# Kernel tuning notes

Hardware: AMD Instinct MI355X
Metric: run time of the kernel (lower is better)

## Reference

```python
import jax, jax.numpy as jnp
import numpy as np

B, T, V, F, O, K_ORDER = 16, 16, 512, 64, 64, 3


def setup_inputs() -> dict:
    key = jax.random.key(0)
    k1, k2, k3, k4 = jax.random.split(key, 4)
    x = jax.random.normal(k1, (B, T, V, F), dtype=jnp.float32)
    Att = jax.random.uniform(k2, (B, V, V), dtype=jnp.float32)
    S = jax.random.uniform(k3, (B, T, V, V), dtype=jnp.float32)
    Theta = jax.random.uniform(k4, (K_ORDER, F, O), dtype=jnp.float32) * 0.1
    return {"x": x, "Att": Att, "S": S, "Theta": Theta}


def reference(x, Att, S, Theta):
    # x: (B,T,V,F); Att: (B,V,V); S: (B,T,V,V); Theta: (k,F,O)
    Bv, Tv, Vv, Fv = x.shape
    k_order = Theta.shape[0]
    # symmetrize via elementwise min with transpose over the two vertex dims
    S = jnp.minimum(S, jnp.swapaxes(S, -1, -2))
    # per-timestep: D = diag(sum(A, axis=1)) (sum over rows, i.e. axis=2 here)
    deg = S.sum(axis=2)                      # (B,T,V)
    eye = jnp.eye(Vv, dtype=x.dtype)
    # L_t = D - A - I
    L_t = deg[..., None] * eye - S - eye     # (B,T,V,V)
    Att_b = Att[:, None]                     # (B,1,V,V) broadcast over T

    # Chebyshev recurrence is ELEMENTWISE in the original code: T_k = 2*L_t*T_{k-1} - T_{k-2}
    Tkm2 = jnp.broadcast_to(eye, L_t.shape)  # T_0 = I
    Tkm1 = L_t                               # T_1 = L_t
    # rhs = (T_k * Att)^T @ x  ->  sum_u (T_k*Att)[u,v] * x[u,f]; then @ Theta[k]
    out = jnp.einsum('btuv,btuf,fo->btvo', Tkm2 * Att_b, x, Theta[0])
    if k_order > 1:
        out = out + jnp.einsum('btuv,btuf,fo->btvo', Tkm1 * Att_b, x, Theta[1])
    for i in range(2, k_order):
        Tk = 2.0 * L_t * Tkm1 - Tkm2
        out = out + jnp.einsum('btuv,btuf,fo->btvo', Tk * Att_b, x, Theta[i])
        Tkm2, Tkm1 = Tkm1, Tk
    return jax.nn.relu(out)                  # (B,T,V,O)
```

## Files before the change

kernel.cpp:

```cpp
#include <hip/hip_runtime.h>

#define VV 512
#define FF 64
#define OO 64
#define YELEMS 8388608

#define C1_OFF    0u
#define C2_OFF    67108864u
#define Y1F8_OFF  134217728u
#define Y2F8_OFF  142606336u
#define YVO_OFF   150994944u
#define DEGP_OFF  201326592u
#define SDG_OFF   205520896u
#define ADG_OFF   206045184u
#define WS_NEED   206569472u

using f32x4  = __attribute__((ext_vector_type(4))) float;
using f32x16 = __attribute__((ext_vector_type(16))) float;
using s16x8  = __attribute__((ext_vector_type(8))) short;
using u16x4  = __attribute__((ext_vector_type(4))) unsigned short;
using i64x2  = __attribute__((ext_vector_type(2))) long;

__device__ __forceinline__ short f2bf(float f) {
    union { float f; unsigned int u; } v; v.f = f;
    unsigned int u = v.u;
    u += 0x7fffu + ((u >> 16) & 1u);
    return (short)(u >> 16);
}
__device__ __forceinline__ float bf2f(unsigned short u) {
    union { unsigned int u; float f; } v; v.u = ((unsigned int)u) << 16; return v.f;
}
__device__ __forceinline__ int swz(int row) { return (row >> 1) & 7; }

__device__ __forceinline__ void gload16(const void* g, void* l) {
    __builtin_amdgcn_global_load_lds(
        (const __attribute__((address_space(1))) unsigned int*)g,
        (__attribute__((address_space(3))) unsigned int*)l, 16, 0, 0);
}

__device__ __forceinline__ void coef_pass(
    const float (*Tuv)[65], const float (*Tvu)[65], const float (*Auv)[65],
    float (*degred)[64], unsigned char* c1row0, unsigned char* c2row0, int u0c,
    int tid, bool isdiag, float* SdgW, float* AdgW)
{
    const int uq = (tid & 15) * 4;
    const int vrow = tid >> 4;
    const int ug = u0c + uq;
    const int s  = ug >> 3;
    const int du = (s & 1) * 256 + (s >> 1) * 8 + (uq & 4);
    float dd0 = 0.f, dd1 = 0.f, dd2 = 0.f, dd3 = 0.f;
    #pragma unroll
    for (int it = 0; it < 4; ++it) {
        const int v = vrow + it * 16;
        float c1v[4], c2v[4];
        #pragma unroll
        for (int e = 0; e < 4; ++e) {
            float sm = fminf(Tuv[uq + e][v], Tvu[v][uq + e]);
            float a  = Auv[uq + e][v];
            if (e == 0) dd0 += sm; else if (e == 1) dd1 += sm;
            else if (e == 2) dd2 += sm; else dd3 += sm;
            float c1 = -a * sm;
            float c2 = (a + a) * (sm * sm);
            if (isdiag && (uq + e == v)) {
                c1 = 0.f; c2 = 0.f;
                SdgW[v] = sm; AdgW[v] = a;
            }
            c1v[e] = c1; c2v[e] = c2;
        }
        int w1 = __builtin_amdgcn_cvt_pk_fp8_f32(c1v[0], c1v[1], 0, false);
        w1     = __builtin_amdgcn_cvt_pk_fp8_f32(c1v[2], c1v[3], w1, true);
        int w2 = __builtin_amdgcn_cvt_pk_fp8_f32(c2v[0], c2v[1], 0, false);
        w2     = __builtin_amdgcn_cvt_pk_fp8_f32(c2v[2], c2v[3], w2, true);
        *(int*)(c1row0 + (size_t)v * VV + du) = w1;
        *(int*)(c2row0 + (size_t)v * VV + du) = w2;
    }
    degred[vrow][uq + 0] = dd0;
    degred[vrow][uq + 1] = dd1;
    degred[vrow][uq + 2] = dd2;
    degred[vrow][uq + 3] = dd3;
}

__global__ __launch_bounds__(256, 2)
void coef_kernel(const float* __restrict__ S, const float* __restrict__ Att,
                 unsigned char* __restrict__ ws)
{
    __shared__ float Tij[64][65];
    __shared__ float Tji[64][65];
    __shared__ float Aij[64][65];
    __shared__ float Aji[64][65];
    __shared__ float degA[16][64];
    __shared__ float degB[16][64];

    const int tid = threadIdx.x;
    const int bt = blockIdx.x / 36;
    int p = blockIdx.x - bt * 36;
    int i = 0;
    while (p >= 8 - i) { p -= 8 - i; ++i; }
    const int j = i + p;
    const int b = bt >> 4;
    const int u0i = i * 64, u0j = j * 64;

    const float* Sbt = S + (size_t)bt * VV * VV;
    const float* Abt = Att + (size_t)b * VV * VV;

    {
        const int r = tid >> 2, c4 = (tid & 3) * 16;
        const float* gij = Sbt + (size_t)(u0i + r) * VV + u0j + c4;
        const float* gji = Sbt + (size_t)(u0j + r) * VV + u0i + c4;
        const float* aij = Abt + (size_t)(u0i + r) * VV + u0j + c4;
        const float* aji = Abt + (size_t)(u0j + r) * VV + u0i + c4;
        #pragma unroll
        for (int w = 0; w < 4; ++w) {
            float4 t = ((const float4*)gij)[w];
            Tij[r][c4 + w * 4 + 0] = t.x; Tij[r][c4 + w * 4 + 1] = t.y;
            Tij[r][c4 + w * 4 + 2] = t.z; Tij[r][c4 + w * 4 + 3] = t.w;
        }
        #pragma unroll
        for (int w = 0; w < 4; ++w) {
            float4 t = ((const float4*)gji)[w];
            Tji[r][c4 + w * 4 + 0] = t.x; Tji[r][c4 + w * 4 + 1] = t.y;
            Tji[r][c4 + w * 4 + 2] = t.z; Tji[r][c4 + w * 4 + 3] = t.w;
        }
        #pragma unroll
        for (int w = 0; w < 4; ++w) {
            float4 t = ((const float4*)aij)[w];
            Aij[r][c4 + w * 4 + 0] = t.x; Aij[r][c4 + w * 4 + 1] = t.y;
            Aij[r][c4 + w * 4 + 2] = t.z; Aij[r][c4 + w * 4 + 3] = t.w;
        }
        #pragma unroll
        for (int w = 0; w < 4; ++w) {
            float4 t = ((const float4*)aji)[w];
            Aji[r][c4 + w * 4 + 0] = t.x; Aji[r][c4 + w * 4 + 1] = t.y;
            Aji[r][c4 + w * 4 + 2] = t.z; Aji[r][c4 + w * 4 + 3] = t.w;
        }
    }
    __syncthreads();

    unsigned char* c1w = ws + C1_OFF + (size_t)bt * (VV * VV);
    unsigned char* c2w = ws + C2_OFF + (size_t)bt * (VV * VV);
    float* SdgW = (float*)(ws + SDG_OFF) + (size_t)bt * VV;
    float* AdgW = (float*)(ws + ADG_OFF) + (size_t)bt * VV;
    float* degpW = (float*)(ws + DEGP_OFF) + (size_t)bt * 8 * VV;

    coef_pass(Tij, Tji, Aij, degA,
              c1w + (size_t)u0j * VV, c2w + (size_t)u0j * VV, u0i,
              tid, (i == j), SdgW + u0j, AdgW + u0j);
    if (i < j) {
        coef_pass(Tji, Tij, Aji, degB,
                  c1w + (size_t)u0i * VV, c2w + (size_t)u0i * VV, u0j,
                  tid, false, SdgW, AdgW);
    }
    __syncthreads();

    if (tid < 64) {
        float s = 0.f;
        #pragma unroll
        for (int k = 0; k < 16; ++k) s += degA[k][tid];
        degpW[(size_t)j * VV + u0i + tid] = s;
    } else if (tid < 128 && i < j) {
        float s = 0.f;
        #pragma unroll
        for (int k = 0; k < 16; ++k) s += degB[k][tid - 64];
        degpW[(size_t)i * VV + u0j + (tid - 64)] = s;
    }
}

__global__ __launch_bounds__(256, 4)
void y_kernel2(const float* __restrict__ x, const float* __restrict__ Theta,
               unsigned char* __restrict__ ws)
{
    __shared__ __align__(16) unsigned char smem[32768];
    short* xT = (short*)(smem);

    const int tid = threadIdx.x, lane = tid & 63, q = tid >> 6;
    const int g = lane >> 4, nbase = lane & 15;
    const int bt = blockIdx.x >> 3;
    const int u0 = (blockIdx.x & 7) * 64;

    {
        const float* xp = x + ((size_t)(bt * VV + u0 + lane)) * FF + q * 16;
        float4 a0 = ((const float4*)xp)[0];
        float4 a1 = ((const float4*)xp)[1];
        float4 a2 = ((const float4*)xp)[2];
        float4 a3 = ((const float4*)xp)[3];
        float v[16] = {a0.x,a0.y,a0.z,a0.w, a1.x,a1.y,a1.z,a1.w,
                       a2.x,a2.y,a2.z,a2.w, a3.x,a3.y,a3.z,a3.w};
        s16x8 p0, p1;
        #pragma unroll
        for (int e = 0; e < 8; ++e) { p0[e] = f2bf(v[e]); p1[e] = f2bf(v[8 + e]); }
        const int fs = swz(lane);
        *(s16x8*)&xT[lane * 64 + (((q * 2)     ^ fs) * 8)] = p0;
        *(s16x8*)&xT[lane * 64 + (((q * 2 + 1) ^ fs) * 8)] = p1;
    }
    #pragma unroll
    for (int k = 0; k < 3; ++k) {
        short* tk = (short*)(smem + 8192 + k * 8192);
        s16x8 p0, p1;
        #pragma unroll
        for (int e = 0; e < 8; ++e) {
            p0[e] = f2bf(Theta[k * FF * OO + (q * 16 + e) * OO + lane]);
            p1[e] = f2bf(Theta[k * FF * OO + (q * 16 + 8 + e) * OO + lane]);
        }
        const int fs = swz(lane);
        *(s16x8*)&tk[lane * 64 + (((q * 2)     ^ fs) * 8)] = p0;
        *(s16x8*)&tk[lane * 64 + (((q * 2 + 1) ^ fs) * 8)] = p1;
    }
    __syncthreads();

    f32x4 zero = {0.f, 0.f, 0.f, 0.f};
    f32x4 acc[3][4];
    #pragma unroll
    for (int k = 0; k < 3; ++k)
        #pragma unroll
        for (int nt = 0; nt < 4; ++nt) acc[k][nt] = zero;

    const int mrow = q * 16 + nbase;
    const int moff = mrow * 64, ms = swz(mrow);
    #pragma unroll
    for (int kk = 0; kk < 2; ++kk) {
        const int slotA = kk * 4 + g;
        s16x8 a = *(const s16x8*)&xT[moff + ((slotA ^ ms) * 8)];
        #pragma unroll
        for (int nt = 0; nt < 4; ++nt) {
            const int nrow = nt * 16 + nbase;
            const int nad = nrow * 64 + ((slotA ^ swz(nrow)) * 8);
            #pragma unroll
            for (int k = 0; k < 3; ++k) {
                s16x8 bb = *(const s16x8*)&((short*)(smem + 8192 + k * 8192))[nad];
                acc[k][nt] = __builtin_amdgcn_mfma_f32_16x16x32_bf16(a, bb, acc[k][nt], 0, 0, 0);
            }
        }
    }
    unsigned short* yvo = (unsigned short*)(ws + YVO_OFF);
    unsigned char* y1f8 = ws + Y1F8_OFF + (size_t)bt * 32768;
    unsigned char* y2f8 = ws + Y2F8_OFF + (size_t)bt * 32768;
    #pragma unroll
    for (int k = 0; k < 3; ++k) {
        #pragma unroll
        for (int nt = 0; nt < 4; ++nt) {
            const int o = nt * 16 + nbase;
            const int u = u0 + q * 16 + g * 4;
            #pragma unroll
            for (int r = 0; r < 4; ++r)
                yvo[(size_t)k * YELEMS + (size_t)bt * 32768 + (size_t)(u + r) * OO + o] =
                    (unsigned short)f2bf(acc[k][nt][r]);
            if (k >= 1) {
                const int s = u >> 3;
                const int sw = (s & ~15) | ((s & 15) ^ (o & 15));
                const int ad = o * 512 + sw * 8 + (u & 4);
                int w = __builtin_amdgcn_cvt_pk_fp8_f32(acc[k][nt][0], acc[k][nt][1], 0, false);
                w     = __builtin_amdgcn_cvt_pk_fp8_f32(acc[k][nt][2], acc[k][nt][3], w, true);
                if (k == 1) *(int*)(y1f8 + ad) = w;
                else        *(int*)(y2f8 + ad) = w;
            }
        }
    }
}

__global__ __launch_bounds__(256, 2)
void cheb_b(const unsigned char* __restrict__ ws, float* __restrict__ out)
{
    __shared__ __align__(16) unsigned char yLds[65536];

    const int tid = threadIdx.x, lane = tid & 63;
    const int wv = tid >> 6;
    const int vh = wv >> 1, oh = wv & 1;
    const int rl = lane & 31, hi = lane >> 5;

    const int wg = blockIdx.x;
    const int bt = (wg & 7) + ((wg >> 6) << 3);
    const int vt = (wg >> 3) & 7;
    const int v0 = vt * 64;

    {
        const unsigned char* y1img = ws + Y1F8_OFF + (size_t)bt * 32768;
        const unsigned char* y2img = ws + Y2F8_OFF + (size_t)bt * 32768;
        const int wo = wv * 1024 + lane * 16;
        #pragma unroll
        for (int i = 0; i < 8; ++i) {
            gload16(y1img + i * 4096 + wo, (char*)yLds + i * 4096 + wv * 1024);
            gload16(y2img + i * 4096 + wo, (char*)yLds + 32768 + i * 4096 + wv * 1024);
        }
    }

    const size_t crow = (size_t)(v0 + vh * 32 + rl) * VV + hi * 256;
    const unsigned char* c1base = ws + C1_OFF + (size_t)bt * (VV * VV) + crow;
    const unsigned char* c2base = ws + C2_OFF + (size_t)bt * (VV * VV) + crow;
    i64x2 c1p[16], c2p[16];
    #pragma unroll
    for (int jj = 0; jj < 16; ++jj) {
        c1p[jj] = *(const i64x2*)(c1base + jj * 16);
        c2p[jj] = *(const i64x2*)(c2base + jj * 16);
    }

    __syncthreads();

    f32x16 acc;
    #pragma unroll
    for (int i = 0; i < 16; ++i) acc[i] = 0.f;

    const int yrow = (oh * 32 + rl) * 512;
    const int x15  = rl & 15;

    #pragma unroll
    for (int it = 0; it < 32; ++it) {
        const long a1 = c1p[it >> 1][it & 1];
        const long a2 = c2p[it >> 1][it & 1];
        const int s  = it * 2 + hi;
        const int sw = (s & ~15) | ((s & 15) ^ x15);
        const int ad = yrow + sw * 8;
        const long b1 = *(const long*)&yLds[ad];
        const long b2 = *(const long*)&yLds[32768 + ad];
        acc = __builtin_amdgcn_mfma_f32_32x32x16_fp8_fp8(a1, b1, acc, 0, 0, 0);
        acc = __builtin_amdgcn_mfma_f32_32x32x16_fp8_fp8(a2, b2, acc, 0, 0, 0);
    }

    __syncthreads();
    {
        float* ep = (float*)yLds;
        const float* degp = (const float*)(ws + DEGP_OFF) + (size_t)bt * 8 * VV;
        const float* SdgW = (const float*)(ws + SDG_OFF) + (size_t)bt * VV;
        const float* AdgW = (const float*)(ws + ADG_OFF) + (size_t)bt * VV;
        if (tid < 64) {
            float dv = 0.f;
            #pragma unroll
            for (int s = 0; s < 8; ++s) dv += degp[(size_t)s * VV + v0 + tid];
            ep[tid] = dv;
        } else if (tid < 128) {
            ep[64 + (tid - 64)] = SdgW[v0 + (tid - 64)];
        } else if (tid < 192) {
            ep[128 + (tid - 128)] = AdgW[v0 + (tid - 128)];
        }
    }
    __syncthreads();

    const float* ep = (const float*)yLds;
    const unsigned short* yvo = (const unsigned short*)(ws + YVO_OFF) + (size_t)bt * 32768;
    float* obt = out + (size_t)bt * VV * OO;
    const int o = oh * 32 + rl;

    #pragma unroll
    for (int r = 0; r < 16; ++r) {
        const int vloc = vh * 32 + (r & 3) + 8 * (r >> 2) + 4 * hi;
        const int vgr = v0 + vloc;
        const float dv = ep[vloc];
        const float Sd = ep[64 + vloc];
        const float Ad = ep[128 + vloc];
        const float Ld = dv - Sd - 1.0f;
        const float w1 = Ad * Ld;
        const float w2 = Ad * (2.0f * Ld * Ld - 1.0f);
        const size_t yi = (size_t)vgr * OO + o;
        float y0v = bf2f(yvo[yi]);
        float y1v = bf2f(yvo[(size_t)YELEMS + yi]);
        float y2v = bf2f(yvo[(size_t)2 * YELEMS + yi]);
        float val = acc[r] + Ad * y0v + w1 * y1v + w2 * y2v;
        obt[(size_t)vgr * OO + o] = fmaxf(val, 0.0f);
    }
}

__global__ __launch_bounds__(256, 4)
void y_kernel_fb(const float* __restrict__ x, const float* __restrict__ Theta,
                 unsigned short* __restrict__ yT)
{
    __shared__ __align__(16) unsigned char smem[32768];
    short* xT = (short*)(smem);
    const int tid = threadIdx.x, lane = tid & 63, q = tid >> 6;
    const int g = lane >> 4, nbase = lane & 15;
    const int bt = blockIdx.x >> 3;
    const int u0 = (blockIdx.x & 7) * 64;
    {
        const float* xp = x + ((size_t)(bt * VV + u0 + lane)) * FF + q * 16;
        float4 a0 = ((const float4*)xp)[0];
        float4 a1 = ((const float4*)xp)[1];
        float4 a2 = ((const float4*)xp)[2];
        float4 a3 = ((const float4*)xp)[3];
        float v[16] = {a0.x,a0.y,a0.z,a0.w, a1.x,a1.y,a1.z,a1.w,
                       a2.x,a2.y,a2.z,a2.w, a3.x,a3.y,a3.z,a3.w};
        s16x8 p0, p1;
        #pragma unroll
        for (int e = 0; e < 8; ++e) { p0[e] = f2bf(v[e]); p1[e] = f2bf(v[8 + e]); }
        const int fs = swz(lane);
        *(s16x8*)&xT[lane * 64 + (((q * 2)     ^ fs) * 8)] = p0;
        *(s16x8*)&xT[lane * 64 + (((q * 2 + 1) ^ fs) * 8)] = p1;
    }
    #pragma unroll
    for (int k = 0; k < 3; ++k) {
        short* tk = (short*)(smem + 8192 + k * 8192);
        s16x8 p0, p1;
        #pragma unroll
        for (int e = 0; e < 8; ++e) {
            p0[e] = f2bf(Theta[k * FF * OO + (q * 16 + e) * OO + lane]);
            p1[e] = f2bf(Theta[k * FF * OO + (q * 16 + 8 + e) * OO + lane]);
        }
        const int fs = swz(lane);
        *(s16x8*)&tk[lane * 64 + (((q * 2)     ^ fs) * 8)] = p0;
        *(s16x8*)&tk[lane * 64 + (((q * 2 + 1) ^ fs) * 8)] = p1;
    }
    __syncthreads();
    f32x4 zero = {0.f, 0.f, 0.f, 0.f};
    f32x4 acc[3][4];
    #pragma unroll
    for (int k = 0; k < 3; ++k)
        #pragma unroll
        for (int nt = 0; nt < 4; ++nt) acc[k][nt] = zero;
    const int mrow = q * 16 + nbase;
    const int moff = mrow * 64, ms = swz(mrow);
    #pragma unroll
    for (int kk = 0; kk < 2; ++kk) {
        const int slotA = kk * 4 + g;
        s16x8 a = *(const s16x8*)&xT[moff + ((slotA ^ ms) * 8)];
        #pragma unroll
        for (int nt = 0; nt < 4; ++nt) {
            const int nrow = nt * 16 + nbase;
            const int nad = nrow * 64 + ((slotA ^ swz(nrow)) * 8);
            #pragma unroll
            for (int k = 0; k < 3; ++k) {
                s16x8 bb = *(const s16x8*)&((short*)(smem + 8192 + k * 8192))[nad];
                acc[k][nt] = __builtin_amdgcn_mfma_f32_16x16x32_bf16(a, bb, acc[k][nt], 0, 0, 0);
            }
        }
    }
    #pragma unroll
    for (int k = 0; k < 3; ++k) {
        #pragma unroll
        for (int nt = 0; nt < 4; ++nt) {
            const int o = nt * 16 + nbase;
            const int u = u0 + q * 16 + g * 4;
            u16x4 pk;
            #pragma unroll
            for (int r = 0; r < 4; ++r) pk[r] = (unsigned short)f2bf(acc[k][nt][r]);
            *(u16x4*)&yT[(size_t)k * YELEMS + ((size_t)(bt * 64 + o)) * VV + u] = pk;
        }
    }
}

__global__ __launch_bounds__(256, 4)
void cheb_main_fb(const float* __restrict__ S, const float* __restrict__ Att,
                  const unsigned short* __restrict__ yT, float* __restrict__ out)
{
    const int tid = threadIdx.x, lane = tid & 63, q = tid >> 6;
    const int g = lane >> 4, nbase = lane & 15;
    const int wg = blockIdx.x;
    const int bt = (wg & 7) + ((wg >> 6) << 3);
    const int vt = (wg >> 3) & 7;
    const int v0 = vt * 64;
    const int b  = bt >> 4;
    const float* Sbt = S + (size_t)bt * VV * VV;
    const float* Abt = Att + (size_t)b * VV * VV;
    const unsigned short* y0g = yT + (size_t)bt * 64 * VV;
    const unsigned short* y1g = y0g + (size_t)YELEMS;
    const unsigned short* y2g = y0g + (size_t)2 * YELEMS;
    const int mrow = q * 16 + nbase;
    const int vg   = v0 + mrow;
    const float* Srow = Sbt + (size_t)vg * VV;
    const float* Scol = Sbt + vg;
    const float* Acol = Abt + vg;
    f32x4 zero = {0.f, 0.f, 0.f, 0.f};
    f32x4 acc[4];
    #pragma unroll
    for (int i = 0; i < 4; ++i) acc[i] = zero;
    float da0 = 0.f, da1 = 0.f, adg = 0.f, sdg = 0.f;
    #pragma unroll
    for (int ut = 0; ut < 8; ++ut) {
        const int u0t = ut * 64;
        #pragma unroll
        for (int kk = 0; kk < 2; ++kk) {
            const int ub = u0t + (kk * 4 + g) * 8;
            s16x8 b10 = *(const s16x8*)&y1g[(size_t)(0 * 16 + nbase) * VV + ub];
            s16x8 b11 = *(const s16x8*)&y1g[(size_t)(1 * 16 + nbase) * VV + ub];
            s16x8 b12 = *(const s16x8*)&y1g[(size_t)(2 * 16 + nbase) * VV + ub];
            s16x8 b13 = *(const s16x8*)&y1g[(size_t)(3 * 16 + nbase) * VV + ub];
            f32x4 r0 = *(const f32x4*)(Srow + ub);
            f32x4 r1 = *(const f32x4*)(Srow + ub + 4);
            s16x8 a1, a2;
            #pragma unroll
            for (int e = 0; e < 8; ++e) {
                float sc = Scol[(size_t)(ub + e) * VV];
                float av = Acol[(size_t)(ub + e) * VV];
                float rv = (e < 4) ? r0[e] : r1[e - 4];
                float sm = fminf(sc, rv);
                if (e & 1) da1 += sm; else da0 += sm;
                float c1 = -av * sm;
                float c2 = (av + av) * (sm * sm);
                if (ub + e == vg) { c1 = 0.f; c2 = 0.f; adg = av; sdg = sm; }
                a1[e] = f2bf(c1);
                a2[e] = f2bf(c2);
            }
            acc[0] = __builtin_amdgcn_mfma_f32_16x16x32_bf16(a1, b10, acc[0], 0, 0, 0);
            acc[1] = __builtin_amdgcn_mfma_f32_16x16x32_bf16(a1, b11, acc[1], 0, 0, 0);
            acc[2] = __builtin_amdgcn_mfma_f32_16x16x32_bf16(a1, b12, acc[2], 0, 0, 0);
            acc[3] = __builtin_amdgcn_mfma_f32_16x16x32_bf16(a1, b13, acc[3], 0, 0, 0);
            s16x8 b20 = *(const s16x8*)&y2g[(size_t)(0 * 16 + nbase) * VV + ub];
            s16x8 b21 = *(const s16x8*)&y2g[(size_t)(1 * 16 + nbase) * VV + ub];
            s16x8 b22 = *(const s16x8*)&y2g[(size_t)(2 * 16 + nbase) * VV + ub];
            s16x8 b23 = *(const s16x8*)&y2g[(size_t)(3 * 16 + nbase) * VV + ub];
            acc[0] = __builtin_amdgcn_mfma_f32_16x16x32_bf16(a2, b20, acc[0], 0, 0, 0);
            acc[1] = __builtin_amdgcn_mfma_f32_16x16x32_bf16(a2, b21, acc[1], 0, 0, 0);
            acc[2] = __builtin_amdgcn_mfma_f32_16x16x32_bf16(a2, b22, acc[2], 0, 0, 0);
            acc[3] = __builtin_amdgcn_mfma_f32_16x16x32_bf16(a2, b23, acc[3], 0, 0, 0);
        }
    }
    float da = da0 + da1;
    da  += __shfl_xor(da, 16);  da  += __shfl_xor(da, 32);
    adg += __shfl_xor(adg, 16); adg += __shfl_xor(adg, 32);
    sdg += __shfl_xor(sdg, 16); sdg += __shfl_xor(sdg, 32);
    float* obt = out + (size_t)bt * VV * OO;
    #pragma unroll
    for (int r = 0; r < 4; ++r) {
        const int vloc = q * 16 + g * 4 + r;
        const int src  = g * 4 + r;
        const float Ad = __shfl(adg, src);
        const float dv = __shfl(da,  src);
        const float Sd = __shfl(sdg, src);
        const float Ld = dv - Sd - 1.0f;
        const float w1 = Ad * Ld;
        const float w2 = Ad * (2.0f * Ld * Ld - 1.0f);
        const int vgr = v0 + vloc;
        #pragma unroll
        for (int nt = 0; nt < 4; ++nt) {
            const int oo = nt * 16 + nbase;
            const size_t yi = (size_t)oo * VV + vgr;
            float y0v = bf2f(y0g[yi]);
            float y1v = bf2f(y1g[yi]);
            float y2v = bf2f(y2g[yi]);
            float val = acc[nt][r] + Ad * y0v + w1 * y1v + w2 * y2v;
            obt[(size_t)vgr * OO + oo] = fmaxf(val, 0.0f);
        }
    }
}

extern "C" void kernel_launch(void* const* d_in, const int* in_sizes, int n_in,
                              void* d_out, int out_size, void* d_ws, size_t ws_size,
                              hipStream_t stream) {
    (void)in_sizes; (void)n_in; (void)out_size;
    const float* x   = (const float*)d_in[0];
    const float* Att = (const float*)d_in[1];
    const float* S   = (const float*)d_in[2];
    const float* Th  = (const float*)d_in[3];
    float* outp = (float*)d_out;
    if (ws_size >= (size_t)WS_NEED) {
        unsigned char* ws = (unsigned char*)d_ws;
        hipLaunchKernelGGL(coef_kernel, dim3(9216), dim3(256), 0, stream, S, Att, ws);
        hipLaunchKernelGGL(y_kernel2, dim3(2048), dim3(256), 0, stream, x, Th, ws);
        hipLaunchKernelGGL(cheb_b, dim3(2048), dim3(256), 0, stream, ws, outp);
    } else {
        unsigned short* yT = (unsigned short*)d_ws;
        hipLaunchKernelGGL(y_kernel_fb, dim3(2048), dim3(256), 0, stream, x, Th, yT);
        hipLaunchKernelGGL(cheb_main_fb, dim3(2048), dim3(256), 0, stream, S, Att, yT, outp);
    }
}
```

Before: 219.2 us.

## Restructure coef kernel: bf16 Att in LDS, 16-byte fp8 stores, shuffle degree reduction

Rewrites the coefficient kernel so the Att tiles are kept in LDS as bf16 instead of fp32, which cuts LDS use and allows a launch bound of three blocks per CU. Each thread now handles one vertex row and packs 16 fp8 coefficients into a single int4 global store, replacing the scattered 4-byte writes. The per-vertex degree partial sums are reduced with warp shuffles rather than an LDS reduction plus an extra barrier, and the diagonal S/Att values are read straight from global memory. Rounding Att to bf16 adds some error before the fp8 quantization.

```diff
diff --git a/kernel.cpp b/kernel.cpp
--- a/kernel.cpp
+++ b/kernel.cpp
@@ -18,6 +18,7 @@
 using f32x4  = __attribute__((ext_vector_type(4))) float;
 using f32x16 = __attribute__((ext_vector_type(16))) float;
 using s16x8  = __attribute__((ext_vector_type(8))) short;
+using s16x4  = __attribute__((ext_vector_type(4))) short;
 using u16x4  = __attribute__((ext_vector_type(4))) unsigned short;
 using i64x2  = __attribute__((ext_vector_type(2))) long;
 
@@ -38,58 +39,14 @@
         (__attribute__((address_space(3))) unsigned int*)l, 16, 0, 0);
 }
 
-__device__ __forceinline__ void coef_pass(
-    const float (*Tuv)[65], const float (*Tvu)[65], const float (*Auv)[65],
-    float (*degred)[64], unsigned char* c1row0, unsigned char* c2row0, int u0c,
-    int tid, bool isdiag, float* SdgW, float* AdgW)
-{
-    const int uq = (tid & 15) * 4;
-    const int vrow = tid >> 4;
-    const int ug = u0c + uq;
-    const int s  = ug >> 3;
-    const int du = (s & 1) * 256 + (s >> 1) * 8 + (uq & 4);
-    float dd0 = 0.f, dd1 = 0.f, dd2 = 0.f, dd3 = 0.f;
-    #pragma unroll
-    for (int it = 0; it < 4; ++it) {
-        const int v = vrow + it * 16;
-        float c1v[4], c2v[4];
-        #pragma unroll
-        for (int e = 0; e < 4; ++e) {
-            float sm = fminf(Tuv[uq + e][v], Tvu[v][uq + e]);
-            float a  = Auv[uq + e][v];
-            if (e == 0) dd0 += sm; else if (e == 1) dd1 += sm;
-            else if (e == 2) dd2 += sm; else dd3 += sm;
-            float c1 = -a * sm;
-            float c2 = (a + a) * (sm * sm);
-            if (isdiag && (uq + e == v)) {
-                c1 = 0.f; c2 = 0.f;
-                SdgW[v] = sm; AdgW[v] = a;
-            }
-            c1v[e] = c1; c2v[e] = c2;
-        }
-        int w1 = __builtin_amdgcn_cvt_pk_fp8_f32(c1v[0], c1v[1], 0, false);
-        w1     = __builtin_amdgcn_cvt_pk_fp8_f32(c1v[2], c1v[3], w1, true);
-        int w2 = __builtin_amdgcn_cvt_pk_fp8_f32(c2v[0], c2v[1], 0, false);
-        w2     = __builtin_amdgcn_cvt_pk_fp8_f32(c2v[2], c2v[3], w2, true);
-        *(int*)(c1row0 + (size_t)v * VV + du) = w1;
-        *(int*)(c2row0 + (size_t)v * VV + du) = w2;
-    }
-    degred[vrow][uq + 0] = dd0;
-    degred[vrow][uq + 1] = dd1;
-    degred[vrow][uq + 2] = dd2;
-    degred[vrow][uq + 3] = dd3;
-}
-
-__global__ __launch_bounds__(256, 2)
+__global__ __launch_bounds__(256, 3)
 void coef_kernel(const float* __restrict__ S, const float* __restrict__ Att,
                  unsigned char* __restrict__ ws)
 {
-    __shared__ float Tij[64][65];
-    __shared__ float Tji[64][65];
-    __shared__ float Aij[64][65];
-    __shared__ float Aji[64][65];
-    __shared__ float degA[16][64];
-    __shared__ float degB[16][64];
+    __shared__ float Sij[64][65];
+    __shared__ float Sji[64][65];
+    __shared__ short Aij[64][68];
+    __shared__ short Aji[64][68];
 
     const int tid = threadIdx.x;
     const int bt = blockIdx.x / 36;
@@ -112,56 +69,91 @@
         #pragma unroll
         for (int w = 0; w < 4; ++w) {
             float4 t = ((const float4*)gij)[w];
-            Tij[r][c4 + w * 4 + 0] = t.x; Tij[r][c4 + w * 4 + 1] = t.y;
-            Tij[r][c4 + w * 4 + 2] = t.z; Tij[r][c4 + w * 4 + 3] = t.w;
+            Sij[r][c4 + w * 4 + 0] = t.x; Sij[r][c4 + w * 4 + 1] = t.y;
+            Sij[r][c4 + w * 4 + 2] = t.z; Sij[r][c4 + w * 4 + 3] = t.w;
         }
         #pragma unroll
         for (int w = 0; w < 4; ++w) {
             float4 t = ((const float4*)gji)[w];
-            Tji[r][c4 + w * 4 + 0] = t.x; Tji[r][c4 + w * 4 + 1] = t.y;
-            Tji[r][c4 + w * 4 + 2] = t.z; Tji[r][c4 + w * 4 + 3] = t.w;
+            Sji[r][c4 + w * 4 + 0] = t.x; Sji[r][c4 + w * 4 + 1] = t.y;
+            Sji[r][c4 + w * 4 + 2] = t.z; Sji[r][c4 + w * 4 + 3] = t.w;
         }
         #pragma unroll
         for (int w = 0; w < 4; ++w) {
             float4 t = ((const float4*)aij)[w];
-            Aij[r][c4 + w * 4 + 0] = t.x; Aij[r][c4 + w * 4 + 1] = t.y;
-            Aij[r][c4 + w * 4 + 2] = t.z; Aij[r][c4 + w * 4 + 3] = t.w;
+            s16x4 pk = { f2bf(t.x), f2bf(t.y), f2bf(t.z), f2bf(t.w) };
+            *(s16x4*)&Aij[r][c4 + w * 4] = pk;
         }
         #pragma unroll
         for (int w = 0; w < 4; ++w) {
             float4 t = ((const float4*)aji)[w];
-            Aji[r][c4 + w * 4 + 0] = t.x; Aji[r][c4 + w * 4 + 1] = t.y;
-            Aji[r][c4 + w * 4 + 2] = t.z; Aji[r][c4 + w * 4 + 3] = t.w;
-        }
+            s16x4 pk = { f2bf(t.x), f2bf(t.y), f2bf(t.z), f2bf(t.w) };
+            *(s16x4*)&Aji[r][c4 + w * 4] = pk;
+        }
+    }
+    if (i == j && tid < 64) {
+        const int vg = u0i + tid;
+        ((float*)(ws + SDG_OFF))[(size_t)bt * VV + vg] = Sbt[(size_t)vg * VV + vg];
+        ((float*)(ws + ADG_OFF))[(size_t)bt * VV + vg] = Abt[(size_t)vg * VV + vg];
     }
     __syncthreads();
 
     unsigned char* c1w = ws + C1_OFF + (size_t)bt * (VV * VV);
     unsigned char* c2w = ws + C2_OFF + (size_t)bt * (VV * VV);
-    float* SdgW = (float*)(ws + SDG_OFF) + (size_t)bt * VV;
-    float* AdgW = (float*)(ws + ADG_OFF) + (size_t)bt * VV;
     float* degpW = (float*)(ws + DEGP_OFF) + (size_t)bt * 8 * VV;
 
-    coef_pass(Tij, Tji, Aij, degA,
-              c1w + (size_t)u0j * VV, c2w + (size_t)u0j * VV, u0i,
-              tid, (i == j), SdgW + u0j, AdgW + u0j);
-    if (i < j) {
-        coef_pass(Tji, Tij, Aji, degB,
-                  c1w + (size_t)u0i * VV, c2w + (size_t)u0i * VV, u0j,
-                  tid, false, SdgW, AdgW);
-    }
-    __syncthreads();
-
-    if (tid < 64) {
-        float s = 0.f;
-        #pragma unroll
-        for (int k = 0; k < 16; ++k) s += degA[k][tid];
-        degpW[(size_t)j * VV + u0i + tid] = s;
-    } else if (tid < 128 && i < j) {
-        float s = 0.f;
-        #pragma unroll
-        for (int k = 0; k < 16; ++k) s += degB[k][tid - 64];
-        degpW[(size_t)i * VV + u0j + (tid - 64)] = s;
+    const int v  = tid >> 2;
+    const int sp = tid & 3;
+    const int pr = sp >> 1, idx = sp & 1;
+
+    #pragma unroll
+    for (int pass = 0; pass < 2; ++pass) {
+        if (pass == 1 && i == j) break;
+        const float (*Tuv)[65] = (pass == 0) ? Sij : Sji;
+        const float (*Tvu)[65] = (pass == 0) ? Sji : Sij;
+        const short (*Auv)[68] = (pass == 0) ? Aij : Aji;
+        const int I = (pass == 0) ? i : j;
+        const int J = (pass == 0) ? j : i;
+        const bool dtile = (i == j);
+
+        float degp = 0.f;
+        int w1[4], w2[4];
+        #pragma unroll
+        for (int t = 0; t < 2; ++t) {
+            const int sl = idx * 4 + t * 2 + pr;
+            float c1v[8], c2v[8];
+            #pragma unroll
+            for (int e = 0; e < 8; ++e) {
+                const int u = sl * 8 + e;
+                float sm = fminf(Tuv[u][v], Tvu[v][u]);
+                float a  = bf2f((unsigned short)Auv[u][v]);
+                degp += sm;
+                float c1 = -a * sm;
+                float c2 = (a + a) * (sm * sm);
+                if (dtile && (u == v)) { c1 = 0.f; c2 = 0.f; }
+                c1v[e] = c1; c2v[e] = c2;
+            }
+            int a0 = __builtin_amdgcn_cvt_pk_fp8_f32(c1v[0], c1v[1], 0, false);
+            a0     = __builtin_amdgcn_cvt_pk_fp8_f32(c1v[2], c1v[3], a0, true);
+            int a1 = __builtin_amdgcn_cvt_pk_fp8_f32(c1v[4], c1v[5], 0, false);
+            a1     = __builtin_amdgcn_cvt_pk_fp8_f32(c1v[6], c1v[7], a1, true);
+            int b0 = __builtin_amdgcn_cvt_pk_fp8_f32(c2v[0], c2v[1], 0, false);
+            b0     = __builtin_amdgcn_cvt_pk_fp8_f32(c2v[2], c2v[3], b0, true);
+            int b1 = __builtin_amdgcn_cvt_pk_fp8_f32(c2v[4], c2v[5], 0, false);
+            b1     = __builtin_amdgcn_cvt_pk_fp8_f32(c2v[6], c2v[7], b1, true);
+            w1[t * 2] = a0; w1[t * 2 + 1] = a1;
+            w2[t * 2] = b0; w2[t * 2 + 1] = b1;
+        }
+        const int vglob = J * 64 + v;
+        const size_t rowoff = (size_t)vglob * VV + pr * 256 + I * 32 + idx * 16;
+        int4 s1 = { w1[0], w1[1], w1[2], w1[3] };
+        int4 s2 = { w2[0], w2[1], w2[2], w2[3] };
+        *(int4*)(c1w + rowoff) = s1;
+        *(int4*)(c2w + rowoff) = s2;
+
+        degp += __shfl_xor(degp, 1);
+        degp += __shfl_xor(degp, 2);
+        if (sp == 0) degpW[(size_t)I * VV + vglob] = degp;
     }
 }
 
```

Result: faster. 214.5 us (-2.2%).
